# Performance work log

Measured on AMD Instinct MI355X. Metric: run time of the kernel, lower is better.

## Reference

```python
import jax, jax.numpy as jnp
import numpy as np

# Concrete FBSNN instance (LQ control): mu=q, sigma=sigma_x*I, f=q^2, g(y)=y^2
SIGMA_X = 0.5
DT = 0.01
ALPHA = 1.0  # terminal cost weight: g(y) = ALPHA * y^2


def _net(Ws, bs, t, y):
    # FCnet([2,64,64,64,64,1]) with Sine activation: Y_net(t, y)
    x = jnp.concatenate([t, y], axis=-1)  # [B, 2]
    for W, b in zip(Ws[:-1], bs[:-1]):
        x = jnp.sin(x @ W.T + b)
    return x @ Ws[-1].T + bs[-1]  # [B, 1]


def setup_inputs() -> dict:
    key = jax.random.key(0)
    dims = [2, 64, 64, 64, 64, 1]
    keys = jax.random.split(key, 12)
    inp = {}
    for i in range(5):
        inp[f"W{i}"] = (jax.random.normal(keys[i], (dims[i + 1], dims[i]), dtype=jnp.float32)
                         / np.float32(np.sqrt(dims[i])))
        inp[f"b{i}"] = jnp.zeros((dims[i + 1],), dtype=jnp.float32)
    inp["y0_param"] = jnp.ones((1,), dtype=jnp.float32)
    # standard normal increments; scaled by sqrt(dt) inside reference (matches torch.randn * dt**0.5)
    inp["dW"] = jax.random.normal(keys[10], (100, 131072, 1), dtype=jnp.float32)
    return inp


def reference(W0, b0, W1, b1, W2, b2, W3, b3, W4, b4, y0_param, dW):
    Ws = [W0, W1, W2, W3, W4]
    bs = [b0, b1, b2, b3, b4]
    B = dW.shape[1]
    sqrt_dt = np.float32(DT) ** 0.5

    def net_and_grad(t, y):
        # Y = Y_net(t, y) and dY/dy per sample (batch is elementwise, so a
        # single vjp with ones cotangent equals torch.autograd.grad w/ ones).
        Y, vjp = jax.vjp(lambda yy: _net(Ws, bs, t, yy), y)
        dY = vjp(jnp.ones_like(Y))[0]
        return Y, dY

    t0 = jnp.zeros((B, 1), dtype=dW.dtype)
    y0 = jnp.tile(y0_param[None, :], (B, 1))  # y0.repeat(batch_size, 1)
    Y0, dY0 = net_and_grad(t0, y0)

    def step(carry, dw):
        t, y0, Y0, dY0, loss = carry
        sig = SIGMA_X                       # sigma(t, y) = sigma_x * I (dim=dim_W=1)
        Z0 = sig * dY0                      # bmm(sigma, dY)  -> [B,1]
        q0 = -0.5 * Z0 / (SIGMA_X ** 2)     # optimal control
        dws = dw * sqrt_dt                  # [B,1]
        y1 = y0 + q0 * DT + sig * dws       # Euler-Maruyama: mu = q
        t1 = t + DT
        Y1, dY1 = net_and_grad(t1, y1)
        f = q0 ** 2                         # generator(y, q) = q^2
        Y1_tilde = Y0 - f * DT + jnp.sum(Z0 * dws, axis=1, keepdims=True)
        loss = loss + jnp.mean((Y1 - Y1_tilde) ** 2)
        return (t1, y1, Y1, dY1, loss), None

    init = (t0, y0, Y0, dY0, jnp.zeros((), dtype=dW.dtype))
    (tN, yN, YN, dYN, y_loss), _ = jax.lax.scan(step, init, dW)

    terminal = ALPHA * yN ** 2              # terminal_cost(y) = y^2, [B,1]
    terminal_loss = jnp.mean((YN - terminal) ** 2)
    terminal_grad = 2.0 * ALPHA * yN        # d/dy of terminal cost
    terminal_grad_loss = jnp.mean((dYN - terminal_grad) ** 2)
    return y_loss + terminal_loss + terminal_grad_loss
```

## Files before the change

### kernel.cpp

```cpp
#include <hip/hip_runtime.h>

#define BATCH  131072
#define NSTEPS 100

typedef _Float16 half8 __attribute__((ext_vector_type(8)));
typedef float    f32x4 __attribute__((ext_vector_type(4)));
typedef unsigned int u32x2 __attribute__((ext_vector_type(2)));
typedef unsigned int u32x4 __attribute__((ext_vector_type(4)));

extern "C" __global__ void __launch_bounds__(256, 5)
fbsnn_kernel(const float* __restrict__ W0, const float* __restrict__ b0,
             const float* __restrict__ W1, const float* __restrict__ b1,
             const float* __restrict__ W2, const float* __restrict__ b2,
             const float* __restrict__ W3, const float* __restrict__ b3,
             const float* __restrict__ W4, const float* __restrict__ b4,
             const float* __restrict__ y0p, const float* __restrict__ dW,
             float* __restrict__ out)
{
    __shared__ _Float16 X[2][8192];
    float* part = (float*)&X[1][0];

    const int tid = threadIdx.x;
    const int l   = tid & 63;
    const int wu  = __builtin_amdgcn_readfirstlane(tid >> 6);
    const int i   = l & 15;
    const int g   = l >> 4;
    const int sample = blockIdx.x * 64 + l;

    const float DT = 0.01f, SQDT = 0.1f;

    half8 afr[3][2];
    const float* Wsrc[3] = {W1, W2, W3};
    #pragma unroll
    for (int li = 0; li < 3; ++li)
        #pragma unroll
        for (int kt = 0; kt < 2; ++kt) {
            const float* wr = Wsrc[li] + (16 * wu + i) * 64 + kt * 32 + g * 8;
            #pragma unroll
            for (int e = 0; e < 8; ++e) afr[li][kt][e] = (_Float16)wr[e];
        }

    const int mrow = 16 * wu + 4 * g;
    float bias[3][4], W4l[4];
    const float* bsrc[3] = {b1, b2, b3};
    #pragma unroll
    for (int li = 0; li < 3; ++li)
        #pragma unroll
        for (int r = 0; r < 4; ++r) bias[li][r] = bsrc[li][mrow + r];
    #pragma unroll
    for (int r = 0; r < 4; ++r) W4l[r] = W4[mrow + r];
    const float b4v = b4[0];

    const int swz  = (i & 7) << 4;
    const int rb0  = i * 128 + ((16 * g) ^ swz);
    const int rb1  = i * 128 + ((64 + 16 * g) ^ swz);
    const int wbx  = i * 128 + ((32 * wu + 8 * g) ^ swz);
    const int swz0 = (l & 7) << 4;
    const int l0a  = l * 128 + ((32 * wu) ^ swz0);
    const int l0b  = l * 128 + ((32 * wu + 16) ^ swz0);

    float y = y0p[0];
    float t = 0.0f;
    float Y0 = 0.f, dY0 = 0.f, q0 = 0.f, Z0 = 0.f, dws = 0.f, loss = 0.f;

    for (int s = 0; s <= NSTEPS; ++s) {
        float dwv = 0.0f;
        if (s < NSTEPS) dwv = dW[s * BATCH + sample];

        {
            u32x4 xlo, xhi, vlo, vhi;
            #pragma unroll
            for (int jj = 0; jj < 8; ++jj) {
                int n0 = 16 * wu + 2 * jj;
                float wa0 = W0[2 * n0 + 0], wb0 = W0[2 * n0 + 1];
                float wa1 = W0[2 * n0 + 2], wb1 = W0[2 * n0 + 3];
                float z0 = fmaf(wa0, t, fmaf(wb0, y, b0[n0 + 0]));
                float z1 = fmaf(wa1, t, fmaf(wb1, y, b0[n0 + 1]));
                float s0, c0, s1, c1;
                __sincosf(z0, &s0, &c0);
                __sincosf(z1, &s1, &c1);
                unsigned xs = __builtin_bit_cast(unsigned, __builtin_amdgcn_cvt_pkrtz(s0, s1));
                unsigned vs = __builtin_bit_cast(unsigned, __builtin_amdgcn_cvt_pkrtz(c0 * wb0, c1 * wb1));
                if (jj < 4) { xlo[jj] = xs; vlo[jj] = vs; }
                else        { xhi[jj - 4] = xs; vhi[jj - 4] = vs; }
            }
            char* Xb = (char*)&X[0][0];
            *(u32x4*)(Xb + l0a)        = xlo;
            *(u32x4*)(Xb + l0b)        = xhi;
            *(u32x4*)(Xb + 8192 + l0a) = vlo;
            *(u32x4*)(Xb + 8192 + l0b) = vhi;
        }
        __syncthreads();

        #pragma unroll
        for (int li = 0; li < 3; ++li) {
            const char* Xr = (const char*)&X[li & 1][0];
            f32x4 ax[4], av[4];
            #pragma unroll
            for (int tt = 0; tt < 4; ++tt) {
                half8 bx0 = *(const half8*)(Xr + rb0 + tt * 2048);
                half8 bx1 = *(const half8*)(Xr + rb1 + tt * 2048);
                f32x4 a = {bias[li][0], bias[li][1], bias[li][2], bias[li][3]};
                a = __builtin_amdgcn_mfma_f32_16x16x32_f16(afr[li][0], bx0, a, 0, 0, 0);
                a = __builtin_amdgcn_mfma_f32_16x16x32_f16(afr[li][1], bx1, a, 0, 0, 0);
                ax[tt] = a;
                half8 bv0 = *(const half8*)(Xr + 8192 + rb0 + tt * 2048);
                half8 bv1 = *(const half8*)(Xr + 8192 + rb1 + tt * 2048);
                f32x4 v = {0.f, 0.f, 0.f, 0.f};
                v = __builtin_amdgcn_mfma_f32_16x16x32_f16(afr[li][0], bv0, v, 0, 0, 0);
                v = __builtin_amdgcn_mfma_f32_16x16x32_f16(afr[li][1], bv1, v, 0, 0, 0);
                av[tt] = v;
            }

            if (li < 2) {
                char* Xw = (char*)&X[(li + 1) & 1][0];
                #pragma unroll
                for (int tt = 0; tt < 4; ++tt) {
                    float sn0, cs0, sn1, cs1, sn2, cs2, sn3, cs3;
                    __sincosf(ax[tt][0], &sn0, &cs0);
                    __sincosf(ax[tt][1], &sn1, &cs1);
                    __sincosf(ax[tt][2], &sn2, &cs2);
                    __sincosf(ax[tt][3], &sn3, &cs3);
                    u32x2 xo, vo;
                    xo[0] = __builtin_bit_cast(unsigned, __builtin_amdgcn_cvt_pkrtz(sn0, sn1));
                    xo[1] = __builtin_bit_cast(unsigned, __builtin_amdgcn_cvt_pkrtz(sn2, sn3));
                    vo[0] = __builtin_bit_cast(unsigned, __builtin_amdgcn_cvt_pkrtz(cs0 * av[tt][0], cs1 * av[tt][1]));
                    vo[1] = __builtin_bit_cast(unsigned, __builtin_amdgcn_cvt_pkrtz(cs2 * av[tt][2], cs3 * av[tt][3]));
                    *(u32x2*)(Xw + wbx + tt * 2048)        = xo;
                    *(u32x2*)(Xw + 8192 + wbx + tt * 2048) = vo;
                }
            } else {
                #pragma unroll
                for (int tt = 0; tt < 4; ++tt) {
                    float sx = 0.f, sv = 0.f;
                    #pragma unroll
                    for (int r = 0; r < 4; ++r) {
                        float sn, cs;
                        __sincosf(ax[tt][r], &sn, &cs);
                        sx = fmaf(W4l[r], sn, sx);
                        sv = fmaf(W4l[r], cs * av[tt][r], sv);
                    }
                    sx += __shfl_xor(sx, 16); sx += __shfl_xor(sx, 32);
                    sv += __shfl_xor(sv, 16); sv += __shfl_xor(sv, 32);
                    if (l < 16) {
                        part[128 * wu + 16 * tt + l]      = sx;
                        part[128 * wu + 64 + 16 * tt + l] = sv;
                    }
                }
            }
            __syncthreads();
        }

        float Y1  = ((part[l] + part[128 + l]) + (part[256 + l] + part[384 + l])) + b4v;
        float dY1 = ((part[64 + l] + part[192 + l]) + (part[320 + l] + part[448 + l]));

        if (s > 0) {
            float Yt = Y0 - q0 * q0 * DT + Z0 * dws;
            float d  = Y1 - Yt;
            loss += d * d;
        }
        Y0 = Y1; dY0 = dY1;
        if (s < NSTEPS) {
            Z0  = 0.5f * dY0;
            q0  = -dY0;
            dws = dwv * SQDT;
            y   = y + q0 * DT + 0.5f * dws;
            t   = t + DT;
        }
    }

    float d1 = Y0 - y * y;
    float d2 = dY0 - 2.0f * y;
    loss += d1 * d1 + d2 * d2;

    if (tid < 64) {
        #pragma unroll
        for (int off = 1; off < 64; off <<= 1)
            loss += __shfl_xor(loss, off);
        if (tid == 0) atomicAdd(out, loss / (float)BATCH);
    }
}

extern "C" void kernel_launch(void* const* d_in, const int* in_sizes, int n_in,
                              void* d_out, int out_size, void* d_ws, size_t ws_size,
                              hipStream_t stream) {
    const float* W0  = (const float*)d_in[0];
    const float* b0  = (const float*)d_in[1];
    const float* W1  = (const float*)d_in[2];
    const float* b1  = (const float*)d_in[3];
    const float* W2  = (const float*)d_in[4];
    const float* b2  = (const float*)d_in[5];
    const float* W3  = (const float*)d_in[6];
    const float* b3  = (const float*)d_in[7];
    const float* W4  = (const float*)d_in[8];
    const float* b4  = (const float*)d_in[9];
    const float* y0p = (const float*)d_in[10];
    const float* dW  = (const float*)d_in[11];
    float* out = (float*)d_out;

    hipMemsetAsync(d_out, 0, sizeof(float), stream);

    dim3 grid(BATCH / 64);
    dim3 block(256);
    fbsnn_kernel<<<grid, block, 0, stream>>>(W0, b0, W1, b1, W2, b2, W3, b3,
                                             W4, b4, y0p, dW, out);
}
```

Measured before the change: 1.104 ms.

## Give each wave its own 16 samples with register-resident activations, dropping shared memory

Before, the four waves of a block split the 64 output neurons and exchanged activations through LDS with a barrier after every layer. Now each wave owns 16 samples and holds the full weight set (4 M-tiles per layer) in registers as fp16 fragments. The MFMA output layout is repacked directly into the next layer's B operand in registers, so shared memory and __syncthreads disappear. Register pressure goes up sharply (launch bounds drop to 2), and each wave computes only 16 samples across 64 lanes, which duplicates the layer-0 sin/cos work and the final-layer reduction work. The final loss is reduced through 256 atomic slots plus a small finish kernel instead of one global atomic.

```diff
diff --git a/kernel.cpp b/kernel.cpp
--- a/kernel.cpp
+++ b/kernel.cpp
@@ -3,156 +3,183 @@
 #define BATCH  131072
 #define NSTEPS 100
 
-typedef _Float16 half8 __attribute__((ext_vector_type(8)));
-typedef float    f32x4 __attribute__((ext_vector_type(4)));
-typedef unsigned int u32x2 __attribute__((ext_vector_type(2)));
-typedef unsigned int u32x4 __attribute__((ext_vector_type(4)));
-
-extern "C" __global__ void __launch_bounds__(256, 5)
+typedef _Float16 half8  __attribute__((ext_vector_type(8)));
+typedef _Float16 half2t __attribute__((ext_vector_type(2)));
+typedef float    f32x4  __attribute__((ext_vector_type(4)));
+typedef unsigned u32x4  __attribute__((ext_vector_type(4)));
+
+__device__ __forceinline__ unsigned pkh2(float a, float b) {
+    return __builtin_bit_cast(unsigned, __builtin_amdgcn_cvt_pkrtz(a, b));
+}
+__device__ __forceinline__ float loh(unsigned u) {
+    half2t h = __builtin_bit_cast(half2t, u); return (float)h[0];
+}
+__device__ __forceinline__ float hih(unsigned u) {
+    half2t h = __builtin_bit_cast(half2t, u); return (float)h[1];
+}
+
+extern "C" __global__ void __launch_bounds__(256, 2)
 fbsnn_kernel(const float* __restrict__ W0, const float* __restrict__ b0,
              const float* __restrict__ W1, const float* __restrict__ b1,
              const float* __restrict__ W2, const float* __restrict__ b2,
              const float* __restrict__ W3, const float* __restrict__ b3,
              const float* __restrict__ W4, const float* __restrict__ b4,
              const float* __restrict__ y0p, const float* __restrict__ dW,
-             float* __restrict__ out)
+             float* __restrict__ slots)
 {
-    __shared__ _Float16 X[2][8192];
-    float* part = (float*)&X[1][0];
-
     const int tid = threadIdx.x;
     const int l   = tid & 63;
-    const int wu  = __builtin_amdgcn_readfirstlane(tid >> 6);
-    const int i   = l & 15;
+    const int wu  = tid >> 6;
+    const int c   = l & 15;
     const int g   = l >> 4;
-    const int sample = blockIdx.x * 64 + l;
+    const int sample = blockIdx.x * 64 + wu * 16 + c;
 
     const float DT = 0.01f, SQDT = 0.1f;
 
-    half8 afr[3][2];
-    const float* Wsrc[3] = {W1, W2, W3};
+    half8 afr[3][4][2];
+    const float* Ws[3] = {W1, W2, W3};
     #pragma unroll
     for (int li = 0; li < 3; ++li)
+      #pragma unroll
+      for (int mt = 0; mt < 4; ++mt)
         #pragma unroll
-        for (int kt = 0; kt < 2; ++kt) {
-            const float* wr = Wsrc[li] + (16 * wu + i) * 64 + kt * 32 + g * 8;
+        for (int kt = 0; kt < 2; ++kt)
+          #pragma unroll
+          for (int qq = 0; qq < 2; ++qq) {
+            f32x4 w4v = *reinterpret_cast<const f32x4*>(
+                Ws[li] + (16 * mt + c) * 64 + 32 * kt + 16 * qq + 4 * g);
             #pragma unroll
-            for (int e = 0; e < 8; ++e) afr[li][kt][e] = (_Float16)wr[e];
-        }
-
-    const int mrow = 16 * wu + 4 * g;
-    float bias[3][4], W4l[4];
-    const float* bsrc[3] = {b1, b2, b3};
+            for (int r = 0; r < 4; ++r)
+                afr[li][mt][kt][4 * qq + r] = (_Float16)w4v[r];
+          }
+
+    unsigned bias_p[3][4][2];
+    const float* bs[3] = {b1, b2, b3};
     #pragma unroll
     for (int li = 0; li < 3; ++li)
-        #pragma unroll
-        for (int r = 0; r < 4; ++r) bias[li][r] = bsrc[li][mrow + r];
-    #pragma unroll
-    for (int r = 0; r < 4; ++r) W4l[r] = W4[mrow + r];
+      #pragma unroll
+      for (int mt = 0; mt < 4; ++mt) {
+        f32x4 bv = *reinterpret_cast<const f32x4*>(bs[li] + 16 * mt + 4 * g);
+        bias_p[li][mt][0] = pkh2(bv[0], bv[1]);
+        bias_p[li][mt][1] = pkh2(bv[2], bv[3]);
+      }
+    unsigned w4_p[4][2];
+    #pragma unroll
+    for (int mt = 0; mt < 4; ++mt) {
+        f32x4 wv = *reinterpret_cast<const f32x4*>(W4 + 16 * mt + 4 * g);
+        w4_p[mt][0] = pkh2(wv[0], wv[1]);
+        w4_p[mt][1] = pkh2(wv[2], wv[3]);
+    }
+    unsigned l0wa[4][2], l0wb[4][2], l0b[4][2];
+    #pragma unroll
+    for (int qi = 0; qi < 4; ++qi) {
+        int n0 = 32 * (qi >> 1) + 16 * (qi & 1) + 4 * g;
+        f32x4 r0 = *reinterpret_cast<const f32x4*>(W0 + 2 * n0);
+        f32x4 r1 = *reinterpret_cast<const f32x4*>(W0 + 2 * n0 + 4);
+        f32x4 bb = *reinterpret_cast<const f32x4*>(b0 + n0);
+        l0wa[qi][0] = pkh2(r0[0], r0[2]);  l0wa[qi][1] = pkh2(r1[0], r1[2]);
+        l0wb[qi][0] = pkh2(r0[1], r0[3]);  l0wb[qi][1] = pkh2(r1[1], r1[3]);
+        l0b[qi][0]  = pkh2(bb[0], bb[1]);  l0b[qi][1]  = pkh2(bb[2], bb[3]);
+    }
     const float b4v = b4[0];
-
-    const int swz  = (i & 7) << 4;
-    const int rb0  = i * 128 + ((16 * g) ^ swz);
-    const int rb1  = i * 128 + ((64 + 16 * g) ^ swz);
-    const int wbx  = i * 128 + ((32 * wu + 8 * g) ^ swz);
-    const int swz0 = (l & 7) << 4;
-    const int l0a  = l * 128 + ((32 * wu) ^ swz0);
-    const int l0b  = l * 128 + ((32 * wu + 16) ^ swz0);
 
     float y = y0p[0];
     float t = 0.0f;
     float Y0 = 0.f, dY0 = 0.f, q0 = 0.f, Z0 = 0.f, dws = 0.f, loss = 0.f;
 
+    #pragma unroll 1
     for (int s = 0; s <= NSTEPS; ++s) {
         float dwv = 0.0f;
         if (s < NSTEPS) dwv = dW[s * BATCH + sample];
 
-        {
-            u32x4 xlo, xhi, vlo, vhi;
+        half8 BX[2], BV[2];
+        #pragma unroll
+        for (int kt = 0; kt < 2; ++kt) {
+            u32x4 ux, uv;
             #pragma unroll
-            for (int jj = 0; jj < 8; ++jj) {
-                int n0 = 16 * wu + 2 * jj;
-                float wa0 = W0[2 * n0 + 0], wb0 = W0[2 * n0 + 1];
-                float wa1 = W0[2 * n0 + 2], wb1 = W0[2 * n0 + 3];
-                float z0 = fmaf(wa0, t, fmaf(wb0, y, b0[n0 + 0]));
-                float z1 = fmaf(wa1, t, fmaf(wb1, y, b0[n0 + 1]));
-                float s0, c0, s1, c1;
-                __sincosf(z0, &s0, &c0);
-                __sincosf(z1, &s1, &c1);
-                unsigned xs = __builtin_bit_cast(unsigned, __builtin_amdgcn_cvt_pkrtz(s0, s1));
-                unsigned vs = __builtin_bit_cast(unsigned, __builtin_amdgcn_cvt_pkrtz(c0 * wb0, c1 * wb1));
-                if (jj < 4) { xlo[jj] = xs; vlo[jj] = vs; }
-                else        { xhi[jj - 4] = xs; vhi[jj - 4] = vs; }
+            for (int qq = 0; qq < 2; ++qq) {
+                int qi = 2 * kt + qq;
+                float sn[4], vv[4];
+                #pragma unroll
+                for (int h = 0; h < 2; ++h) {
+                    float wa0 = loh(l0wa[qi][h]), wa1 = hih(l0wa[qi][h]);
+                    float wb0 = loh(l0wb[qi][h]), wb1 = hih(l0wb[qi][h]);
+                    float c00 = loh(l0b[qi][h]),  c01 = hih(l0b[qi][h]);
+                    float z0 = fmaf(wa0, t, fmaf(wb0, y, c00));
+                    float z1 = fmaf(wa1, t, fmaf(wb1, y, c01));
+                    float s0, cc0, s1, cc1;
+                    __sincosf(z0, &s0, &cc0);
+                    __sincosf(z1, &s1, &cc1);
+                    sn[2 * h] = s0; sn[2 * h + 1] = s1;
+                    vv[2 * h] = cc0 * wb0; vv[2 * h + 1] = cc1 * wb1;
+                }
+                ux[2 * qq + 0] = pkh2(sn[0], sn[1]);
+                ux[2 * qq + 1] = pkh2(sn[2], sn[3]);
+                uv[2 * qq + 0] = pkh2(vv[0], vv[1]);
+                uv[2 * qq + 1] = pkh2(vv[2], vv[3]);
             }
-            char* Xb = (char*)&X[0][0];
-            *(u32x4*)(Xb + l0a)        = xlo;
-            *(u32x4*)(Xb + l0b)        = xhi;
-            *(u32x4*)(Xb + 8192 + l0a) = vlo;
-            *(u32x4*)(Xb + 8192 + l0b) = vhi;
-        }
-        __syncthreads();
-
+            BX[kt] = __builtin_bit_cast(half8, ux);
+            BV[kt] = __builtin_bit_cast(half8, uv);
+        }
+
+        float Y1 = 0.f, dY1 = 0.f;
         #pragma unroll
         for (int li = 0; li < 3; ++li) {
-            const char* Xr = (const char*)&X[li & 1][0];
             f32x4 ax[4], av[4];
             #pragma unroll
-            for (int tt = 0; tt < 4; ++tt) {
-                half8 bx0 = *(const half8*)(Xr + rb0 + tt * 2048);
-                half8 bx1 = *(const half8*)(Xr + rb1 + tt * 2048);
-                f32x4 a = {bias[li][0], bias[li][1], bias[li][2], bias[li][3]};
-                a = __builtin_amdgcn_mfma_f32_16x16x32_f16(afr[li][0], bx0, a, 0, 0, 0);
-                a = __builtin_amdgcn_mfma_f32_16x16x32_f16(afr[li][1], bx1, a, 0, 0, 0);
-                ax[tt] = a;
-                half8 bv0 = *(const half8*)(Xr + 8192 + rb0 + tt * 2048);
-                half8 bv1 = *(const half8*)(Xr + 8192 + rb1 + tt * 2048);
+            for (int mt = 0; mt < 4; ++mt) {
+                f32x4 ci;
+                ci[0] = loh(bias_p[li][mt][0]); ci[1] = hih(bias_p[li][mt][0]);
+                ci[2] = loh(bias_p[li][mt][1]); ci[3] = hih(bias_p[li][mt][1]);
+                f32x4 a = __builtin_amdgcn_mfma_f32_16x16x32_f16(afr[li][mt][0], BX[0], ci, 0, 0, 0);
+                a = __builtin_amdgcn_mfma_f32_16x16x32_f16(afr[li][mt][1], BX[1], a, 0, 0, 0);
+                ax[mt] = a;
                 f32x4 v = {0.f, 0.f, 0.f, 0.f};
-                v = __builtin_amdgcn_mfma_f32_16x16x32_f16(afr[li][0], bv0, v, 0, 0, 0);
-                v = __builtin_amdgcn_mfma_f32_16x16x32_f16(afr[li][1], bv1, v, 0, 0, 0);
-                av[tt] = v;
+                v = __builtin_amdgcn_mfma_f32_16x16x32_f16(afr[li][mt][0], BV[0], v, 0, 0, 0);
+                v = __builtin_amdgcn_mfma_f32_16x16x32_f16(afr[li][mt][1], BV[1], v, 0, 0, 0);
+                av[mt] = v;
             }
-
             if (li < 2) {
-                char* Xw = (char*)&X[(li + 1) & 1][0];
+                u32x4 nx[2], nv[2];
                 #pragma unroll
-                for (int tt = 0; tt < 4; ++tt) {
-                    float sn0, cs0, sn1, cs1, sn2, cs2, sn3, cs3;
-                    __sincosf(ax[tt][0], &sn0, &cs0);
-                    __sincosf(ax[tt][1], &sn1, &cs1);
-                    __sincosf(ax[tt][2], &sn2, &cs2);
-                    __sincosf(ax[tt][3], &sn3, &cs3);
-                    u32x2 xo, vo;
-                    xo[0] = __builtin_bit_cast(unsigned, __builtin_amdgcn_cvt_pkrtz(sn0, sn1));
-                    xo[1] = __builtin_bit_cast(unsigned, __builtin_amdgcn_cvt_pkrtz(sn2, sn3));
-                    vo[0] = __builtin_bit_cast(unsigned, __builtin_amdgcn_cvt_pkrtz(cs0 * av[tt][0], cs1 * av[tt][1]));
-                    vo[1] = __builtin_bit_cast(unsigned, __builtin_amdgcn_cvt_pkrtz(cs2 * av[tt][2], cs3 * av[tt][3]));
-                    *(u32x2*)(Xw + wbx + tt * 2048)        = xo;
-                    *(u32x2*)(Xw + 8192 + wbx + tt * 2048) = vo;
-                }
-            } else {
-                #pragma unroll
-                for (int tt = 0; tt < 4; ++tt) {
-                    float sx = 0.f, sv = 0.f;
+                for (int mt = 0; mt < 4; ++mt) {
+                    float sn[4], vv[4];
                     #pragma unroll
                     for (int r = 0; r < 4; ++r) {
-                        float sn, cs;
-                        __sincosf(ax[tt][r], &sn, &cs);
-                        sx = fmaf(W4l[r], sn, sx);
-                        sv = fmaf(W4l[r], cs * av[tt][r], sv);
+                        float s1, c1;
+                        __sincosf(ax[mt][r], &s1, &c1);
+                        sn[r] = s1; vv[r] = c1 * av[mt][r];
                     }
-                    sx += __shfl_xor(sx, 16); sx += __shfl_xor(sx, 32);
-                    sv += __shfl_xor(sv, 16); sv += __shfl_xor(sv, 32);
-                    if (l < 16) {
-                        part[128 * wu + 16 * tt + l]      = sx;
-                        part[128 * wu + 64 + 16 * tt + l] = sv;
+                    nx[mt >> 1][2 * (mt & 1) + 0] = pkh2(sn[0], sn[1]);
+                    nx[mt >> 1][2 * (mt & 1) + 1] = pkh2(sn[2], sn[3]);
+                    nv[mt >> 1][2 * (mt & 1) + 0] = pkh2(vv[0], vv[1]);
+                    nv[mt >> 1][2 * (mt & 1) + 1] = pkh2(vv[2], vv[3]);
+                }
+                BX[0] = __builtin_bit_cast(half8, nx[0]);
+                BX[1] = __builtin_bit_cast(half8, nx[1]);
+                BV[0] = __builtin_bit_cast(half8, nv[0]);
+                BV[1] = __builtin_bit_cast(half8, nv[1]);
+            } else {
+                float sx = 0.f, sv = 0.f;
+                #pragma unroll
+                for (int mt = 0; mt < 4; ++mt) {
+                    float w0 = loh(w4_p[mt][0]), w1 = hih(w4_p[mt][0]);
+                    float w2 = loh(w4_p[mt][1]), w3 = hih(w4_p[mt][1]);
+                    float wv[4] = {w0, w1, w2, w3};
+                    #pragma unroll
+                    for (int r = 0; r < 4; ++r) {
+                        float s1, c1;
+                        __sincosf(ax[mt][r], &s1, &c1);
+                        sx = fmaf(wv[r], s1, sx);
+                        sv = fmaf(wv[r], c1 * av[mt][r], sv);
                     }
                 }
+                sx += __shfl_xor(sx, 16); sx += __shfl_xor(sx, 32);
+                sv += __shfl_xor(sv, 16); sv += __shfl_xor(sv, 32);
+                Y1  = sx + b4v;
+                dY1 = sv;
             }
-            __syncthreads();
-        }
-
-        float Y1  = ((part[l] + part[128 + l]) + (part[256 + l] + part[384 + l])) + b4v;
-        float dY1 = ((part[64 + l] + part[192 + l]) + (part[320 + l] + part[448 + l]));
+        }
 
         if (s > 0) {
             float Yt = Y0 - q0 * q0 * DT + Z0 * dws;
@@ -173,12 +200,22 @@
     float d2 = dY0 - 2.0f * y;
     loss += d1 * d1 + d2 * d2;
 
-    if (tid < 64) {
-        #pragma unroll
-        for (int off = 1; off < 64; off <<= 1)
-            loss += __shfl_xor(loss, off);
-        if (tid == 0) atomicAdd(out, loss / (float)BATCH);
-    }
+    float lv = (g == 0) ? loss : 0.0f;
+    #pragma unroll
+    for (int off = 1; off < 64; off <<= 1)
+        lv += __shfl_xor(lv, off);
+    if (l == 0)
+        atomicAdd(&slots[(blockIdx.x * 4 + wu) & 255], lv);
+}
+
+extern "C" __global__ void finish_kernel(const float* __restrict__ slots,
+                                         float* __restrict__ out) {
+    int l = threadIdx.x;
+    float v = slots[l] + slots[64 + l] + slots[128 + l] + slots[192 + l];
+    #pragma unroll
+    for (int off = 1; off < 64; off <<= 1)
+        v += __shfl_xor(v, off);
+    if (l == 0) out[0] = v * (1.0f / (float)BATCH);
 }
 
 extern "C" void kernel_launch(void* const* d_in, const int* in_sizes, int n_in,
@@ -196,12 +233,13 @@
     const float* b4  = (const float*)d_in[9];
     const float* y0p = (const float*)d_in[10];
     const float* dW  = (const float*)d_in[11];
-    float* out = (float*)d_out;
-
-    hipMemsetAsync(d_out, 0, sizeof(float), stream);
+    float* slots = (float*)d_ws;
+
+    hipMemsetAsync(d_ws, 0, 256 * sizeof(float), stream);
 
     dim3 grid(BATCH / 64);
     dim3 block(256);
     fbsnn_kernel<<<grid, block, 0, stream>>>(W0, b0, W1, b1, W2, b2, W3, b3,
-                                             W4, b4, y0p, dW, out);
-}
+                                             W4, b4, y0p, dW, slots);
+    finish_kernel<<<1, 64, 0, stream>>>(slots, (float*)d_out);
+}
```

After: 987.9 us. -10.5%, faster.
